# Performance work log

Hardware: AMD Instinct MI355X
Metric: run time of the kernel (lower is better)

## Reference

```python
import jax, jax.numpy as jnp
import numpy as np

HEADS = 8
DIM_HEAD = 64
SCALE = DIM_HEAD ** -0.5


def setup_inputs() -> dict:
    key = jax.random.key(0)
    ks = jax.random.split(key, 6)
    B, T, C, H, W = 16, 64, 512, 64, 64
    inner = HEADS * DIM_HEAD  # 512
    return {
        "vision_feature": jax.random.normal(ks[0], (B, C, H, W), jnp.float32),
        "language_feature": jax.random.normal(ks[1], (B, T, C), jnp.float32),
        "mask": jnp.ones((B, T), jnp.int32),  # unused by the module's forward
        "Wq": jax.random.normal(ks[2], (inner, C), jnp.float32) * (C ** -0.5),
        "Wk": jax.random.normal(ks[3], (inner, C), jnp.float32) * (C ** -0.5),
        "Wv": jax.random.normal(ks[4], (inner, C), jnp.float32) * (C ** -0.5),
        "Wo": jax.random.normal(ks[5], (C, inner), jnp.float32) * (inner ** -0.5),
    }


def reference(vision_feature, language_feature, mask, Wq, Wk, Wv, Wo):
    B, T, C = language_feature.shape
    _, _, H, W = vision_feature.shape
    S = H * W
    # 1x1 conv projections == matmuls over the channel dim
    q = jnp.einsum('btc,ic->bti', language_feature, Wq)           # (B, T, inner)
    vis = vision_feature.reshape(B, C, S)                          # (B, C, S)
    k = jnp.einsum('ic,bcs->bis', Wk, vis)                         # (B, inner, S)
    v = jnp.einsum('ic,bcs->bis', Wv, vis)                         # (B, inner, S)
    # split heads: channel index = n*dim_head + d  (n outermost)
    q = q.reshape(B, T, HEADS, DIM_HEAD).transpose(2, 0, 1, 3)     # (h, B, T, d)
    k = k.reshape(B, HEADS, DIM_HEAD, S).transpose(1, 0, 2, 3)     # (h, B, d, S)
    v = v.reshape(B, HEADS, DIM_HEAD, S).transpose(1, 0, 3, 2)     # (h, B, S, d)
    att = jax.nn.softmax(jnp.einsum('hbtd,hbds->hbts', q, k) * SCALE, axis=-1)
    out = jnp.einsum('hbts,hbsd->hbtd', att, v)                    # (h, B, T, d)
    # merge heads back: b (n c) tokens -> equivalently (B, T, h*d)
    out = out.transpose(1, 2, 0, 3).reshape(B, T, HEADS * DIM_HEAD)
    out = jnp.einsum('bti,oi->bto', out, Wo)                       # (B, T, C)
    return out
```

## Files before the change

### kernel.cpp

```cpp
#include <hip/hip_runtime.h>
#include <stdint.h>

typedef __attribute__((ext_vector_type(8))) short short8;
typedef __attribute__((ext_vector_type(4))) short short4v;
typedef __attribute__((ext_vector_type(4))) float float4v;
typedef __attribute__((ext_vector_type(2))) unsigned int uint2v;
typedef __attribute__((ext_vector_type(4))) unsigned int uint4v;
typedef __attribute__((ext_vector_type(8))) __bf16 bf16x8;

#define NCH 4

__device__ __forceinline__ float4v mfma16x16x32(short8 a, short8 b, float4v c) {
  return __builtin_amdgcn_mfma_f32_16x16x32_bf16(
      __builtin_bit_cast(bf16x8, a), __builtin_bit_cast(bf16x8, b), c, 0, 0, 0);
}

__device__ __forceinline__ short f2bf(float f) {
  uint32_t u = __builtin_bit_cast(uint32_t, f);
  u += 0x7fffu + ((u >> 16) & 1u);
  return (short)(u >> 16);
}

__device__ __forceinline__ float bf2f(short s) {
  return __builtin_bit_cast(float, ((uint32_t)(uint16_t)s) << 16);
}

__device__ __forceinline__ uint32_t cvt_pk_bf16(float a, float b) {
  uint32_t r;
  asm("v_cvt_pk_bf16_f32 %0, %1, %2" : "=v"(r) : "v"(a), "v"(b));
  return r;
}

__device__ __forceinline__ void load_lds16(const short* g, short* l) {
  __builtin_amdgcn_global_load_lds(
      (const __attribute__((address_space(1))) void*)g,
      (__attribute__((address_space(3))) void*)l, 16, 0, 0);
}

__global__ __launch_bounds__(256) void convert5(
    const float* __restrict__ sl, short* __restrict__ dl,
    const float* __restrict__ s1, short* __restrict__ d1,
    const float* __restrict__ s2, short* __restrict__ d2,
    const float* __restrict__ s3, short* __restrict__ d3,
    const float* __restrict__ s4, short* __restrict__ d4) {
  const float* src; short* dst; int n4;
  switch (blockIdx.y) {
    case 0: src = sl; dst = dl; n4 = 131072; break;
    case 1: src = s1; dst = d1; n4 = 65536; break;
    case 2: src = s2; dst = d2; n4 = 65536; break;
    case 3: src = s3; dst = d3; n4 = 65536; break;
    default: src = s4; dst = d4; n4 = 65536; break;
  }
  const int stride = gridDim.x * blockDim.x;
  for (int i = blockIdx.x * blockDim.x + threadIdx.x; i < n4; i += stride) {
    float4v v = *(const float4v*)(src + (long)i * 4);
    short4v o;
#pragma unroll
    for (int r = 0; r < 4; r++) o[r] = f2bf(v[r]);
    *(short4v*)(dst + (long)i * 4) = o;
  }
}

template <int OUT_F32>
__global__ __launch_bounds__(256) void gemm_nt(
    const short* __restrict__ A, const short* __restrict__ B,
    void* __restrict__ C, int K, int ldc, float scale) {
  __shared__ alignas(16) short smem[24576];
  const int tid = threadIdx.x;
  const int lane = tid & 63, w = tid >> 6;
  const int quad = lane >> 4, l16 = lane & 15;
  const int wm = w >> 1, wn = w & 1;
  const long m0 = (long)blockIdx.y * 128, n0 = (long)blockIdx.x * 128;

  float4v acc[4][4];
#pragma unroll
  for (int i = 0; i < 4; i++)
#pragma unroll
    for (int j = 0; j < 4; j++) acc[i][j] = (float4v)0.0f;

  const int srow = tid >> 2;
  const int scol = (((tid & 3) ^ ((srow >> 1) & 3))) * 8;
  const int nit = K >> 5;

#define STAGE_NT(t, base)                                                       \
  do {                                                                          \
    load_lds16(&A[(m0 + srow) * K + (t) * 32 + scol], &smem[(base) + tid * 8]); \
    load_lds16(&A[(m0 + 64 + srow) * K + (t) * 32 + scol],                      \
               &smem[(base) + 2048 + tid * 8]);                                 \
    load_lds16(&B[(n0 + srow) * K + (t) * 32 + scol],                           \
               &smem[(base) + 4096 + tid * 8]);                                 \
    load_lds16(&B[(n0 + 64 + srow) * K + (t) * 32 + scol],                      \
               &smem[(base) + 6144 + tid * 8]);                                 \
  } while (0)

  STAGE_NT(0, 0);
  if (nit > 1) STAGE_NT(1, 8192);

  for (int it = 0; it < nit; ++it) {
    const int base = (it % 3) * 8192;
    if (it + 1 < nit) asm volatile("s_waitcnt vmcnt(4)" ::: "memory");
    else              asm volatile("s_waitcnt vmcnt(0)" ::: "memory");
    __builtin_amdgcn_s_barrier();

    if (it + 2 < nit) STAGE_NT(it + 2, ((it + 2) % 3) * 8192);

    const short* lA = &smem[base];
    const short* lB = &smem[base + 4096];
    short8 af[4], bf[4];
#pragma unroll
    for (int t = 0; t < 4; t++) {
      const int ra = wm * 64 + t * 16 + l16;
      const int rb = wn * 64 + t * 16 + l16;
      af[t] = *(const short8*)&lA[ra * 32 + ((quad ^ ((ra >> 1) & 3)) * 8)];
      bf[t] = *(const short8*)&lB[rb * 32 + ((quad ^ ((rb >> 1) & 3)) * 8)];
    }
    __builtin_amdgcn_s_setprio(1);
#pragma unroll
    for (int i = 0; i < 4; i++)
#pragma unroll
      for (int j = 0; j < 4; j++)
        acc[i][j] = mfma16x16x32(af[i], bf[j], acc[i][j]);
    __builtin_amdgcn_s_setprio(0);
  }
#undef STAGE_NT

  const int cm = wm * 64 + quad * 4;
  const int cn = wn * 64 + l16;
  if (OUT_F32) {
    float* Cf = (float*)C;
#pragma unroll
    for (int i = 0; i < 4; i++)
#pragma unroll
      for (int j = 0; j < 4; j++) {
        const long gn = n0 + cn + j * 16;
#pragma unroll
        for (int r = 0; r < 4; r++)
          Cf[(m0 + cm + i * 16 + r) * (long)ldc + gn] = acc[i][j][r] * scale;
      }
  } else {
    short* Cs = (short*)C;
#pragma unroll
    for (int i = 0; i < 4; i++)
#pragma unroll
      for (int j = 0; j < 4; j++) {
        const long gn = n0 + cn + j * 16;
#pragma unroll
        for (int r = 0; r < 4; r++)
          Cs[(m0 + cm + i * 16 + r) * (long)ldc + gn] = f2bf(acc[i][j][r] * scale);
      }
  }
}

__global__ __launch_bounds__(512, 4) void gemm_kv(
    const short* __restrict__ Wk, const short* __restrict__ Wv,
    const float* __restrict__ visf, long sV,
    short* __restrict__ kout, short* __restrict__ vout, long sKV) {
  __shared__ alignas(16) short smem[36864];
  const int tid = threadIdx.x;
  const int lane = tid & 63, w = tid >> 6;
  const int quad = lane >> 4, l16 = lane & 15;
  const int role = w >> 2;
  const int wq = w & 3, wm = wq >> 1, wn = wq & 1;
  const long n0 = (long)blockIdx.x * 128;
  const long m0 = (long)blockIdx.y * 128;
  const float* vis = visf + blockIdx.z * sV;
  short* kz = kout + blockIdx.z * sKV;
  short* vz = vout + blockIdx.z * sKV;

  float4v acc[4][4];
#pragma unroll
  for (int i = 0; i < 4; i++)
#pragma unroll
    for (int j = 0; j < 4; j++) acc[i][j] = (float4v)0.0f;

  const int srow = tid >> 2;
  const int scol = (((tid & 3) ^ ((srow >> 1) & 3))) * 8;
  const short* gWk = &Wk[(m0 + srow) * 512 + scol];
  const short* gWv = &Wv[(m0 + srow) * 512 + scol];

  const int sl = tid & 127;
  const int oct = tid >> 7;
  const float* gv = vis + (long)(oct * 8) * 4096 + n0 + sl;
  const int woff = 8192 + sl * 32 + ((oct ^ ((sl >> 1) & 3)) * 8);

#define STAGE_W(t, base)                                          \
  do {                                                            \
    load_lds16(gWk + (t) * 32, &smem[(base) + tid * 8]);          \
    load_lds16(gWv + (t) * 32, &smem[(base) + 4096 + tid * 8]);   \
  } while (0)

#define VLOAD(t)                                                  \
  do {                                                            \
    _Pragma("unroll")                                             \
    for (int j = 0; j < 8; j++)                                   \
      vf[j] = gv[((t) * 32 + j) * 4096];                          \
  } while (0)

#define VWRITE(base)                                              \
  do {                                                            \
    uint4v pw;                                                    \
    pw.x = cvt_pk_bf16(vf[0], vf[1]);                             \
    pw.y = cvt_pk_bf16(vf[2], vf[3]);                             \
    pw.z = cvt_pk_bf16(vf[4], vf[5]);                             \
    pw.w = cvt_pk_bf16(vf[6], vf[7]);                             \
    *(uint4v*)&smem[(base) + woff] = pw;                          \
  } while (0)

  float vf[8];
  VLOAD(0);
  asm volatile("s_waitcnt vmcnt(0)" ::: "memory");
  VWRITE(0);
  VLOAD(1);
  __builtin_amdgcn_sched_barrier(0);
  STAGE_W(0, 0);
  STAGE_W(1, 12288);

  for (int it = 0; it < 16; ++it) {
    const int base = (it % 3) * 12288;
    if (it < 15) asm volatile("s_waitcnt vmcnt(2)" ::: "memory");
    else         asm volatile("s_waitcnt vmcnt(0)" ::: "memory");
    if (it < 15) VWRITE(((it + 1) % 3) * 12288);
    asm volatile("s_waitcnt lgkmcnt(0)" ::: "memory");
    __builtin_amdgcn_s_barrier();

    if (it + 2 < 16) {
      VLOAD(it + 2);
      __builtin_amdgcn_sched_barrier(0);
      STAGE_W(it + 2, ((it + 2) % 3) * 12288);
    }

    const short* lW = &smem[base + (role ? 4096 : 0)];
    const short* lVis = &smem[base + 8192];
    short8 af[4], bf[4];
#pragma unroll
    for (int t = 0; t < 4; t++) {
      const int ra = wm * 64 + t * 16 + l16;
      const int rb = wn * 64 + t * 16 + l16;
      af[t] = *(const short8*)&lW[ra * 32 + ((quad ^ ((ra >> 1) & 3)) * 8)];
      bf[t] = *(const short8*)&lVis[rb * 32 + ((quad ^ ((rb >> 1) & 3)) * 8)];
    }
    __builtin_amdgcn_s_setprio(1);
#pragma unroll
    for (int i = 0; i < 4; i++)
#pragma unroll
      for (int j = 0; j < 4; j++)
        acc[i][j] = mfma16x16x32(af[i], bf[j], acc[i][j]);
    __builtin_amdgcn_s_setprio(0);
  }
#undef STAGE_W
#undef VLOAD
#undef VWRITE

  const int cm = wm * 64 + quad * 4;
  const int cn = wn * 64 + l16;

  if (role == 1) {
#pragma unroll
    for (int i = 0; i < 4; i++)
#pragma unroll
      for (int j = 0; j < 4; j++) {
        const long gn = n0 + cn + j * 16;
#pragma unroll
        for (int r = 0; r < 4; r++)
          vz[(m0 + cm + i * 16 + r) * 4096 + gn] = f2bf(acc[i][j][r]);
      }
  }

  short* scratch = smem;
#pragma unroll
  for (int h = 0; h < 2; h++) {
    __syncthreads();
    if (role == 0 && wn == h) {
#pragma unroll
      for (int j = 0; j < 4; j++)
#pragma unroll
        for (int i = 0; i < 4; i++) {
          const int nloc = j * 16 + l16;
          const int m = wm * 64 + i * 16 + quad * 4;
          short4v pk;
#pragma unroll
          for (int r = 0; r < 4; r++) pk[r] = f2bf(acc[i][j][r]);
          *(short4v*)&scratch[nloc * 136 + m] = pk;
        }
    }
    __syncthreads();
    {
      const int row = tid >> 3;
      const int off = (tid & 7) * 16;
      short8 v0 = *(const short8*)&scratch[row * 136 + off];
      short8 v1 = *(const short8*)&scratch[row * 136 + off + 8];
      *(short8*)&kz[(n0 + h * 64 + row) * 512 + m0 + off] = v0;
      *(short8*)&kz[(n0 + h * 64 + row) * 512 + m0 + off + 8] = v1;
    }
  }
}

__global__ __launch_bounds__(256) void attn_part(
    const short* __restrict__ q, const short* __restrict__ kws,
    const short* __restrict__ vws, float* __restrict__ Opart,
    float* __restrict__ lpart, int b0) {
  const int h = blockIdx.x;
  const int bz = blockIdx.y;
  const int ch = blockIdx.z;
  const int tid = threadIdx.x;
  const int lane = tid & 63, w = tid >> 6;
  const int quad = lane >> 4, l16 = lane & 15;

  __shared__ alignas(16) short lq[64 * 64];
  __shared__ alignas(16) short lk[128 * 64];
  __shared__ alignas(16) short lv[64 * 128];
  __shared__ alignas(16) short lp[64 * 128];
  __shared__ float lsum[64];

  const short* qb = q + ((long)(b0 + bz) * 64) * 512 + h * 64;
  const short* kb = kws + (long)bz * 4096 * 512 + h * 64;
  const short* vb = vws + (long)bz * 512 * 4096 + (long)h * 64 * 4096;

  if (tid < 64) lsum[tid] = 0.0f;
  {
    const int qr = tid >> 3;
    const int qc = ((tid & 7) ^ (qr & 7)) * 8;
    load_lds16(&qb[qr * 512 + qc], &lq[tid * 8]);
    load_lds16(&qb[(32 + qr) * 512 + qc], &lq[2048 + tid * 8]);
  }
  const int s0_first = ch * (4096 / NCH);
  const int send = s0_first + (4096 / NCH);
#pragma unroll
  for (int it = 0; it < 4; it++) {
    const int li = tid + it * 256;
    const int kr = li >> 3;
    const int kc = ((li & 7) ^ (kr & 7)) * 8;
    load_lds16(&kb[(long)(s0_first + kr) * 512 + kc], &lk[li * 8]);
  }
#pragma unroll
  for (int it = 0; it < 4; it++) {
    const int li = tid + it * 256;
    const int vr = li >> 4;
    const int vc = ((li & 15) ^ (vr & 7)) * 8;
    load_lds16(&vb[(long)vr * 4096 + s0_first + vc], &lv[li * 8]);
  }
  __syncthreads();

  short8 aq[4][2];
#pragma unroll
  for (int mt = 0; mt < 4; mt++)
#pragma unroll
    for (int ks = 0; ks < 2; ks++) {
      const int ra = mt * 16 + l16;
      aq[mt][ks] = *(const short8*)&lq[ra * 64 + (((ks * 4 + quad) ^ (ra & 7)) * 8)];
    }

  float4v osc[4];
#pragma unroll
  for (int mt = 0; mt < 4; mt++) osc[mt] = (float4v)0.0f;
  float lrow[4] = {0.0f, 0.0f, 0.0f, 0.0f};

  const int cbase = w * 4 + (quad >> 1);
  const int sub = (quad & 1) * 4;

  for (int s0 = s0_first; s0 < send; s0 += 128) {
    short8 bk[2][2];
#pragma unroll
    for (int ks = 0; ks < 2; ks++)
#pragma unroll
      for (int si = 0; si < 2; si++) {
        const int rb = (2 * w + si) * 16 + l16;
        bk[ks][si] = *(const short8*)&lk[rb * 64 + (((ks * 4 + quad) ^ (rb & 7)) * 8)];
      }
    short8 bv[4];
#pragma unroll
    for (int ks = 0; ks < 4; ks++) {
      const int rv = w * 16 + l16;
      bv[ks] = *(const short8*)&lv[rv * 128 + (((ks * 4 + quad) ^ (rv & 7)) * 8)];
    }
    __syncthreads();

    if (s0 + 128 < send) {
#pragma unroll
      for (int it = 0; it < 4; it++) {
        const int li = tid + it * 256;
        const int kr = li >> 3;
        const int kc = ((li & 7) ^ (kr & 7)) * 8;
        load_lds16(&kb[(long)(s0 + 128 + kr) * 512 + kc], &lk[li * 8]);
      }
#pragma unroll
      for (int it = 0; it < 4; it++) {
        const int li = tid + it * 256;
        const int vr = li >> 4;
        const int vc = ((li & 15) ^ (vr & 7)) * 8;
        load_lds16(&vb[(long)vr * 4096 + s0 + 128 + vc], &lv[li * 8]);
      }
    }

    float4v sc[2][4];
#pragma unroll
    for (int si = 0; si < 2; si++)
#pragma unroll
      for (int tj = 0; tj < 4; tj++) sc[si][tj] = (float4v)0.0f;
#pragma unroll
    for (int ks = 0; ks < 2; ks++)
#pragma unroll
      for (int si = 0; si < 2; si++)
#pragma unroll
        for (int tj = 0; tj < 4; tj++)
          sc[si][tj] = mfma16x16x32(bk[ks][si], aq[tj][ks], sc[si][tj]);

#pragma unroll
    for (int si = 0; si < 2; si++) {
      const int c = cbase + si * 2;
#pragma unroll
      for (int tj = 0; tj < 4; tj++) {
        float p0 = __expf(fminf(fmaxf(sc[si][tj][0], -80.0f), 30.0f));
        float p1 = __expf(fminf(fmaxf(sc[si][tj][1], -80.0f), 30.0f));
        float p2 = __expf(fminf(fmaxf(sc[si][tj][2], -80.0f), 30.0f));
        float p3 = __expf(fminf(fmaxf(sc[si][tj][3], -80.0f), 30.0f));
        const uint32_t u01 = cvt_pk_bf16(p0, p1);
        const uint32_t u23 = cvt_pk_bf16(p2, p3);
        lrow[tj] += __builtin_bit_cast(float, u01 << 16) +
                    __builtin_bit_cast(float, u01 & 0xffff0000u) +
                    __builtin_bit_cast(float, u23 << 16) +
                    __builtin_bit_cast(float, u23 & 0xffff0000u);
        const int t = tj * 16 + l16;
        uint2v val; val.x = u01; val.y = u23;
        *(uint2v*)&lp[t * 128 + ((c ^ (t & 7)) * 8) + sub] = val;
      }
    }
    asm volatile("s_waitcnt lgkmcnt(0)" ::: "memory");
    __builtin_amdgcn_sched_barrier(0);
    __builtin_amdgcn_s_barrier();

#pragma unroll
    for (int ks = 0; ks < 4; ks++)
#pragma unroll
      for (int mt = 0; mt < 4; mt++) {
        const int rp = mt * 16 + l16;
        const short8 ap = *(const short8*)&lp[rp * 128 + (((ks * 4 + quad) ^ (rp & 7)) * 8)];
        osc[mt] = mfma16x16x32(ap, bv[ks], osc[mt]);
      }
    __syncthreads();
  }

#pragma unroll
  for (int tj = 0; tj < 4; tj++) {
    float v = lrow[tj];
    v += __shfl_xor(v, 16);
    v += __shfl_xor(v, 32);
    if (quad == 0) atomicAdd(&lsum[tj * 16 + l16], v);
  }
  __syncthreads();

  const long bh = bz * 8 + h;
  float* op = Opart + ((bh * NCH + ch) * 64) * 64 + w * 16 + l16;
#pragma unroll
  for (int mt = 0; mt < 4; mt++)
#pragma unroll
    for (int r = 0; r < 4; r++)
      op[(long)(mt * 16 + quad * 4 + r) * 64] = osc[mt][r];
  if (tid < 64) lpart[(bh * NCH + ch) * 64 + tid] = lsum[tid];
}

__global__ __launch_bounds__(256) void attn_combine(
    const float* __restrict__ Opart, const float* __restrict__ lpart,
    short* __restrict__ tmp, int b0, int nbh) {
  const int total4 = nbh * 1024;
  for (int i4 = blockIdx.x * 256 + threadIdx.x; i4 < total4;
       i4 += gridDim.x * 256) {
    const int bh = i4 >> 10;
    const int td = (i4 & 1023) << 2;
    const int t = td >> 6;
    float4v o = (float4v)0.0f;
    float l = 0.0f;
#pragma unroll
    for (int c = 0; c < NCH; c++) {
      o += *(const float4v*)&Opart[(((long)bh * NCH + c) << 12) + td];
      l += lpart[(bh * NCH + c) * 64 + t];
    }
    const float inv = 1.0f / l;
    const int b = b0 + (bh >> 3), h = bh & 7;
    short4v r;
#pragma unroll
    for (int j = 0; j < 4; j++) r[j] = f2bf(o[j] * inv);
    *(short4v*)&tmp[((long)b * 64 + t) * 512 + h * 64 + (td & 63)] = r;
  }
}

extern "C" void kernel_launch(void* const* d_in, const int* in_sizes, int n_in,
                              void* d_out, int out_size, void* d_ws, size_t ws_size,
                              hipStream_t stream) {
  (void)in_sizes; (void)n_in; (void)out_size;
  const float* vis = (const float*)d_in[0];
  const float* lang = (const float*)d_in[1];
  const float* Wq = (const float*)d_in[3];
  const float* Wk = (const float*)d_in[4];
  const float* Wv = (const float*)d_in[5];
  const float* Wo = (const float*)d_in[6];
  float* out = (float*)d_out;

  char* ws = (char*)d_ws;
  const size_t MB = 1 << 20;
  short* q_ws = (short*)(ws + 0 * MB);
  short* tmp_ws = (short*)(ws + 1 * MB);
  short* langb = (short*)(ws + 2 * MB);
  short* Wqb = (short*)(ws + 3 * MB);
  short* Wkb = (short*)(ws + 3 * MB + 512 * 1024);
  short* Wvb = (short*)(ws + 4 * MB);
  short* Wob = (short*)(ws + 4 * MB + 512 * 1024);
  char* grp = ws + 5 * MB;

  const long batch_elems = 4096l * 512;
  const long vis_f32 = 512l * 4096;
  int g = 16;
  const int cands[5] = {1, 2, 4, 8, 16};
  for (int ci = 0; ci < 5; ci++) {
    const int Bgc = 16 / cands[ci];
    const size_t need = 5 * MB + 2ull * Bgc * batch_elems * 2
                        + (size_t)Bgc * 8 * NCH * 4096 * 4
                        + (size_t)Bgc * 8 * NCH * 64 * 4 + 4096;
    if (need <= ws_size) { g = cands[ci]; break; }
  }
  const int Bg = 16 / g;
  short* k_ws = (short*)grp;
  short* v_ws = k_ws + (long)Bg * batch_elems;
  float* Opart = (float*)(v_ws + (long)Bg * batch_elems);
  float* lptr = Opart + (long)Bg * 8 * NCH * 4096;

  convert5<<<dim3(128, 5), 256, 0, stream>>>(lang, langb, Wq, Wqb, Wk, Wkb,
                                             Wv, Wvb, Wo, Wob);

  gemm_nt<0><<<dim3(4, 8), 256, 0, stream>>>(langb, Wqb, q_ws, 512, 512, 0.125f);

  for (int gi = 0; gi < g; gi++) {
    const int b0 = gi * Bg;
    gemm_kv<<<dim3(32, 4, Bg), 512, 0, stream>>>(Wkb, Wvb, vis + (long)b0 * vis_f32,
                                                 vis_f32, k_ws, v_ws, batch_elems);
    attn_part<<<dim3(8, Bg, NCH), 256, 0, stream>>>(q_ws, k_ws, v_ws, Opart, lptr, b0);
    attn_combine<<<512, 256, 0, stream>>>(Opart, lptr, tmp_ws, b0, Bg * 8);
  }

  gemm_nt<1><<<dim3(4, 8), 256, 0, stream>>>(tmp_ws, Wob, out, 512, 512, 1.0f);
}
```

Before: 327.9 us.

## Deepen vision prefetch to two register sets, load Q directly, raise MFMA priority

The K/V projection kernel now double-buffers the fp32 vision loads in two register arrays. It prefetches four stages ahead instead of two, with the main loop fully unrolled and the waitcnt thresholds adjusted, to hide more global-load latency. The attention kernel drops the Q staging through LDS and loads Q fragments straight from global memory into registers, which also removes one LDS buffer. It wraps its MFMA blocks in s_setprio so matrix work gets issue priority. The extra register set and the full unroll raise VGPR pressure and could lower occupancy.

```diff
diff --git a/kernel.cpp b/kernel.cpp
--- a/kernel.cpp
+++ b/kernel.cpp
@@ -189,44 +189,57 @@
     load_lds16(gWv + (t) * 32, &smem[(base) + 4096 + tid * 8]);   \
   } while (0)
 
-#define VLOAD(t)                                                  \
+#define VLOAD(dst, t)                                             \
   do {                                                            \
     _Pragma("unroll")                                             \
     for (int j = 0; j < 8; j++)                                   \
-      vf[j] = gv[((t) * 32 + j) * 4096];                          \
+      dst[j] = gv[((t) * 32 + j) * 4096];                         \
   } while (0)
 
-#define VWRITE(base)                                              \
+#define VWRITE(src, base)                                         \
   do {                                                            \
     uint4v pw;                                                    \
-    pw.x = cvt_pk_bf16(vf[0], vf[1]);                             \
-    pw.y = cvt_pk_bf16(vf[2], vf[3]);                             \
-    pw.z = cvt_pk_bf16(vf[4], vf[5]);                             \
-    pw.w = cvt_pk_bf16(vf[6], vf[7]);                             \
+    pw.x = cvt_pk_bf16(src[0], src[1]);                           \
+    pw.y = cvt_pk_bf16(src[2], src[3]);                           \
+    pw.z = cvt_pk_bf16(src[4], src[5]);                           \
+    pw.w = cvt_pk_bf16(src[6], src[7]);                           \
     *(uint4v*)&smem[(base) + woff] = pw;                          \
   } while (0)
 
-  float vf[8];
-  VLOAD(0);
+  float vfa[8], vfb[8];
+  VLOAD(vfa, 0);
+  VLOAD(vfb, 1);
   asm volatile("s_waitcnt vmcnt(0)" ::: "memory");
-  VWRITE(0);
-  VLOAD(1);
+  VWRITE(vfa, 0);
+  VWRITE(vfb, 12288);
+  VLOAD(vfa, 2);
   __builtin_amdgcn_sched_barrier(0);
   STAGE_W(0, 0);
+  __builtin_amdgcn_sched_barrier(0);
+  VLOAD(vfb, 3);
+  __builtin_amdgcn_sched_barrier(0);
   STAGE_W(1, 12288);
 
+#pragma unroll
   for (int it = 0; it < 16; ++it) {
     const int base = (it % 3) * 12288;
-    if (it < 15) asm volatile("s_waitcnt vmcnt(2)" ::: "memory");
-    else         asm volatile("s_waitcnt vmcnt(0)" ::: "memory");
-    if (it < 15) VWRITE(((it + 1) % 3) * 12288);
-    asm volatile("s_waitcnt lgkmcnt(0)" ::: "memory");
+    if (it <= 12)      asm volatile("s_waitcnt vmcnt(10) lgkmcnt(0)" ::: "memory");
+    else if (it <= 14) asm volatile("s_waitcnt vmcnt(2) lgkmcnt(0)" ::: "memory");
+    else               asm volatile("s_waitcnt vmcnt(0) lgkmcnt(0)" ::: "memory");
     __builtin_amdgcn_s_barrier();
 
     if (it + 2 < 16) {
-      VLOAD(it + 2);
+      if ((it & 1) == 0) VWRITE(vfa, ((it + 2) % 3) * 12288);
+      else               VWRITE(vfb, ((it + 2) % 3) * 12288);
+    }
+    if (it + 4 < 16) {
+      if ((it & 1) == 0) VLOAD(vfa, it + 4);
+      else               VLOAD(vfb, it + 4);
       __builtin_amdgcn_sched_barrier(0);
+    }
+    if (it + 2 < 16) {
       STAGE_W(it + 2, ((it + 2) % 3) * 12288);
+      __builtin_amdgcn_sched_barrier(0);
     }
 
     const short* lW = &smem[base + (role ? 4096 : 0)];
@@ -306,7 +319,6 @@
   const int lane = tid & 63, w = tid >> 6;
   const int quad = lane >> 4, l16 = lane & 15;
 
-  __shared__ alignas(16) short lq[64 * 64];
   __shared__ alignas(16) short lk[128 * 64];
   __shared__ alignas(16) short lv[64 * 128];
   __shared__ alignas(16) short lp[64 * 128];
@@ -317,12 +329,6 @@
   const short* vb = vws + (long)bz * 512 * 4096 + (long)h * 64 * 4096;
 
   if (tid < 64) lsum[tid] = 0.0f;
-  {
-    const int qr = tid >> 3;
-    const int qc = ((tid & 7) ^ (qr & 7)) * 8;
-    load_lds16(&qb[qr * 512 + qc], &lq[tid * 8]);
-    load_lds16(&qb[(32 + qr) * 512 + qc], &lq[2048 + tid * 8]);
-  }
   const int s0_first = ch * (4096 / NCH);
   const int send = s0_first + (4096 / NCH);
 #pragma unroll
@@ -339,16 +345,16 @@
     const int vc = ((li & 15) ^ (vr & 7)) * 8;
     load_lds16(&vb[(long)vr * 4096 + s0_first + vc], &lv[li * 8]);
   }
+
+  short8 aq[4][2];
+#pragma unroll
+  for (int mt = 0; mt < 4; mt++)
+#pragma unroll
+    for (int ks = 0; ks < 2; ks++)
+      aq[mt][ks] =
+          *(const short8*)&qb[(mt * 16 + l16) * 512 + (ks * 4 + quad) * 8];
+
   __syncthreads();
-
-  short8 aq[4][2];
-#pragma unroll
-  for (int mt = 0; mt < 4; mt++)
-#pragma unroll
-    for (int ks = 0; ks < 2; ks++) {
-      const int ra = mt * 16 + l16;
-      aq[mt][ks] = *(const short8*)&lq[ra * 64 + (((ks * 4 + quad) ^ (ra & 7)) * 8)];
-    }
 
   float4v osc[4];
 #pragma unroll
@@ -397,6 +403,7 @@
     for (int si = 0; si < 2; si++)
 #pragma unroll
       for (int tj = 0; tj < 4; tj++) sc[si][tj] = (float4v)0.0f;
+    __builtin_amdgcn_s_setprio(1);
 #pragma unroll
     for (int ks = 0; ks < 2; ks++)
 #pragma unroll
@@ -404,6 +411,7 @@
 #pragma unroll
         for (int tj = 0; tj < 4; tj++)
           sc[si][tj] = mfma16x16x32(bk[ks][si], aq[tj][ks], sc[si][tj]);
+    __builtin_amdgcn_s_setprio(0);
 
 #pragma unroll
     for (int si = 0; si < 2; si++) {
@@ -429,6 +437,7 @@
     __builtin_amdgcn_sched_barrier(0);
     __builtin_amdgcn_s_barrier();
 
+    __builtin_amdgcn_s_setprio(1);
 #pragma unroll
     for (int ks = 0; ks < 4; ks++)
 #pragma unroll
@@ -437,6 +446,7 @@
         const short8 ap = *(const short8*)&lp[rp * 128 + (((ks * 4 + quad) ^ (rp & 7)) * 8)];
         osc[mt] = mfma16x16x32(ap, bv[ks], osc[mt]);
       }
+    __builtin_amdgcn_s_setprio(0);
     __syncthreads();
   }
 
```

After: 490.2 us. +49.5%, slower.
